# Kernel tuning notes

Hardware: AMD Instinct MI355X
Metric: run time of the kernel (lower is better)

Reference implementation:

```python
import jax, jax.numpy as jnp
import numpy as np

# Model dims (GatedAttentionLayer of Qwen3.5 ANE hybrid stack)
C = 2048      # hidden_size
H = 16        # num_attention_heads
HK = 4        # num_key_value_heads
D = 128       # head_dim
ROT = 32      # rotary_dim = head_dim * partial_rotary_factor (0.25)
S = 1024      # sequence length (prefill)
CTX = 1024    # kv cache context length
N_ATTN = 6    # number of full-attention layers -> kv_cache leading dim 2*N_ATTN
EPS = 1e-6
ROPE_THETA = 1e7


def _rotate_half(x):
    h = x.shape[-1] // 2
    return jnp.concatenate([-x[..., h:], x[..., :h]], axis=-1)


def _rms_norm(x, w, eps=EPS):
    # Qwen3.5 convention: stored weight is (w - 1), applied as (1 + weight)
    r = jax.lax.rsqrt(jnp.mean(x * x, axis=-1, keepdims=True) + eps)
    return x * r * (1.0 + w)


def setup_inputs() -> dict:
    key = jax.random.key(0)
    ks = jax.random.split(key, 6)
    hidden_states = jax.random.normal(ks[0], (1, C, 1, S), jnp.float32)
    q_proj_w = jax.random.normal(ks[1], (H * 2 * D, C), jnp.float32) * 0.02  # q + gate
    k_proj_w = jax.random.normal(ks[2], (HK * D, C), jnp.float32) * 0.02
    v_proj_w = jax.random.normal(ks[3], (HK * D, C), jnp.float32) * 0.02
    o_proj_w = jax.random.normal(ks[4], (C, H * D), jnp.float32) * 0.02
    q_norm_w = jnp.zeros((D,), jnp.float32)
    k_norm_w = jnp.zeros((D,), jnp.float32)
    kv_cache = jnp.zeros((2 * N_ATTN, HK, CTX, D), jnp.float32)
    position_ids = jnp.arange(S, dtype=jnp.int32)
    # causal mask: 0 on/below diagonal, -1e9 above
    causal_mask = jnp.where(
        jnp.arange(CTX)[None, :] <= jnp.arange(S)[:, None], 0.0, -1e9
    ).astype(jnp.float32)[None, None]  # [1,1,S,CTX]
    # RoPE tables over rotary_dim
    inv_freq = 1.0 / (ROPE_THETA ** (jnp.arange(0, ROT, 2, dtype=jnp.float32) / ROT))
    t = jnp.arange(CTX, dtype=jnp.float32)
    freqs = jnp.outer(t, inv_freq)          # [CTX, ROT//2]
    emb = jnp.concatenate([freqs, freqs], -1)  # [CTX, ROT]
    cos_cached = jnp.cos(emb)
    sin_cached = jnp.sin(emb)
    return dict(hidden_states=hidden_states, q_proj_w=q_proj_w, k_proj_w=k_proj_w,
                v_proj_w=v_proj_w, o_proj_w=o_proj_w, q_norm_w=q_norm_w,
                k_norm_w=k_norm_w, kv_cache=kv_cache, causal_mask=causal_mask,
                position_ids=position_ids, cos_cached=cos_cached,
                sin_cached=sin_cached, attn_layer_idx=0)


def reference(hidden_states, q_proj_w, k_proj_w, v_proj_w, o_proj_w,
              q_norm_w, k_norm_w, kv_cache, causal_mask, position_ids,
              cos_cached, sin_cached, attn_layer_idx):
    x = hidden_states[0, :, 0, :]                     # [C, S]
    q_raw = q_proj_w @ x                              # [H*2D, S]  (1x1 Conv2d == GEMM)
    qg = q_raw.reshape(H, 2 * D, S)
    q = jnp.transpose(qg[:, :D, :], (0, 2, 1))        # [H, S, D]
    gate = jnp.transpose(qg[:, D:, :], (0, 2, 1))     # [H, S, D]
    k = jnp.transpose((k_proj_w @ x).reshape(HK, D, S), (0, 2, 1))  # [HK, S, D]
    v = jnp.transpose((v_proj_w @ x).reshape(HK, D, S), (0, 2, 1))  # [HK, S, D]

    q = _rms_norm(q, q_norm_w)
    k = _rms_norm(k, k_norm_w)

    cos = cos_cached[position_ids]   # [S, ROT]
    sin = sin_cached[position_ids]

    def rope(t):
        rot, pas = t[..., :ROT], t[..., ROT:]
        rot = rot * cos + _rotate_half(rot) * sin
        return jnp.concatenate([rot, pas], axis=-1)

    q, k = rope(q), rope(k)

    # prefill cache write at pos_start = position_ids[0]
    k_idx = 2 * attn_layer_idx
    v_idx = k_idx + 1
    pos_start = position_ids[0]
    kv_cache = jax.lax.dynamic_update_slice(kv_cache, k[None], (k_idx, 0, pos_start, 0))
    kv_cache = jax.lax.dynamic_update_slice(kv_cache, v[None], (v_idx, 0, pos_start, 0))

    g = H // HK  # GQA repeat (expand+reshape == contiguous repeat)
    k_full = jnp.repeat(kv_cache[k_idx], g, axis=0)   # [H, CTX, D]
    v_full = jnp.repeat(kv_cache[v_idx], g, axis=0)   # [H, CTX, D]

    scale = D ** -0.5
    attn = jnp.einsum('hsd,htd->hst', q, k_full) * scale + causal_mask[0]
    attn = jax.nn.softmax(attn, axis=-1)
    out = jnp.einsum('hst,htd->hsd', attn, v_full)    # [H, S, D]
    out = out * jax.nn.sigmoid(gate)
    out = jnp.transpose(out, (0, 2, 1)).reshape(H * D, S)
    output = (o_proj_w @ out)[None, :, None, :]       # [1, C, 1, S]
    return output
```

## Files before the change

kernel.cpp:

```cpp
#include <hip/hip_runtime.h>
#include <cstdint>

#define S_LEN 1024
#define C_DIM 2048
#define NH    16
#define NHK   4
#define HD    128
#define ROT   32
#define SCALE 0.08838834764831845f

typedef __bf16 bf16x8 __attribute__((ext_vector_type(8)));
typedef float floatx4 __attribute__((ext_vector_type(4)));
typedef float floatx16 __attribute__((ext_vector_type(16)));
typedef unsigned short ushortx8 __attribute__((ext_vector_type(8)));

__device__ __forceinline__ unsigned short f2bf(float f) {
  union { float f; uint32_t u; } x; x.f = f;
  uint32_t r = (x.u + 0x7fffu + ((x.u >> 16) & 1u)) >> 16;
  return (unsigned short)r;
}
__device__ __forceinline__ float bf2f(unsigned short v) {
  union { uint32_t u; float f; } x; x.u = (uint32_t)v << 16; return x.f;
}

__device__ __forceinline__ void async_copy16(const unsigned short* g, unsigned short* l) {
  __builtin_amdgcn_global_load_lds(
      (const __attribute__((address_space(1))) void*)g,
      (__attribute__((address_space(3))) void*)l,
      16, 0, 0);
}

#define WAIT_VM(N) asm volatile("s_waitcnt vmcnt(" #N ")" ::: "memory")

__device__ __forceinline__ void bar_lds_only() {
  asm volatile("s_waitcnt lgkmcnt(0)" ::: "memory");
  __builtin_amdgcn_s_barrier();
}

__device__ __forceinline__ int swz8(int row) { return (row ^ (row >> 3)) & 7; }

__global__ __launch_bounds__(256)
void prep_kernel(const float* __restrict__ qw, const float* __restrict__ kw,
                 const float* __restrict__ vw, const float* __restrict__ ow,
                 unsigned short* __restrict__ wout,
                 const float* __restrict__ x, unsigned short* __restrict__ xT) {
  __shared__ float t[32][33];
  int bid = blockIdx.x;
  if (bid < 14336) {
    const int NQ = 4096 * 2048 / 4, NK = 512 * 2048 / 4, NV = 512 * 2048 / 4;
    int i = bid * 256 + threadIdx.x;
    const float* src; int j;
    if (i < NQ) { src = qw; j = i; }
    else if (i < NQ + NK) { src = kw; j = i - NQ; }
    else if (i < NQ + NK + NV) { src = vw; j = i - NQ - NK; }
    else { src = ow; j = i - NQ - NK - NV; }
    float4 v = ((const float4*)src)[j];
    ushort4 o;
    o.x = f2bf(v.x); o.y = f2bf(v.y); o.z = f2bf(v.z); o.w = f2bf(v.w);
    ((ushort4*)wout)[i] = o;
  } else {
    int b2 = bid - 14336;
    int st = b2 & 31, ct = b2 >> 5;
    int c = threadIdx.x & 31, rq = threadIdx.x >> 5;
#pragma unroll
    for (int i = 0; i < 4; ++i) {
      int r = rq + i * 8;
      t[r][c] = x[(size_t)(ct * 32 + r) * S_LEN + st * 32 + c];
    }
    __syncthreads();
#pragma unroll
    for (int i = 0; i < 4; ++i) {
      int r = rq + i * 8;
      xT[(size_t)(st * 32 + r) * C_DIM + ct * 32 + c] = f2bf(t[c][r]);
    }
  }
}

__device__ __forceinline__ void norm_rope_epi4(
    floatx16 (&acc)[2], float (*pp)[64],
    const float* __restrict__ w, const int* __restrict__ pos_ids,
    const float* __restrict__ cosc, const float* __restrict__ sinc,
    unsigned short* __restrict__ outp,
    int wave, int lane, int wm, int scol0) {
  int l31 = lane & 31, half = lane >> 5;
#pragma unroll
  for (int ni = 0; ni < 2; ++ni) {
    float s = 0.f;
#pragma unroll
    for (int reg = 0; reg < 16; ++reg) { float v = acc[ni][reg]; s += v * v; }
    s += __shfl_xor(s, 32);
    if (half == 0) pp[wave][ni * 32 + l31] = s;
  }
  __syncthreads();
#pragma unroll
  for (int ni = 0; ni < 2; ++ni) {
    int ci = ni * 32 + l31;
    float tot = pp[0][ci] + pp[1][ci] + pp[2][ci] + pp[3][ci];
    float rn = rsqrtf(tot * (1.0f / 128.0f) + 1e-6f);
    int scol = scol0 + ni * 32 + l31;
    int pos = pos_ids[scol];
    bool rope = (wm == 0);
#pragma unroll
    for (int g = 0; g < 4; ++g) {
      int dbase = wm + half * 4 + g * 8;
      ushort4 o;
#pragma unroll
      for (int rr = 0; rr < 4; ++rr) {
        int reg = g * 4 + rr;
        int d = dbase + rr;
        float v = acc[ni][reg] * rn * (1.0f + w[d]);
        if (rope) {
          float cv = cosc[pos * ROT + d], sv = sinc[pos * ROT + d];
          int d2 = (d < 16) ? d + 16 : d - 16;
          float pv = acc[ni][reg ^ 8] * rn * (1.0f + w[d2]);
          v = v * cv + ((d < 16) ? -pv : pv) * sv;
        }
        ((unsigned short*)&o)[rr] = f2bf(v);
      }
      *(ushort4*)&outp[(size_t)scol * HD + dbase] = o;
    }
  }
}

#define STAGE_QKV4(B_, KT)                                                     \
  { _Pragma("unroll")                                                          \
    for (int i = 0; i < 4; ++i) {                                              \
      int row = wm + i * 8 + sr;                                               \
      async_copy16(Ag + (size_t)row * C_DIM + (KT) + (sc ^ swz8(row)) * 8,     \
                   &Asm[B_][(wm + i * 8) * 64]);                               \
    }                                                                          \
    _Pragma("unroll")                                                          \
    for (int i = 0; i < 2; ++i) {                                              \
      int row = wave * 16 + i * 8 + sr;                                        \
      async_copy16(Bg + (size_t)row * C_DIM + (KT) + (sc ^ swz8(row)) * 8,     \
                   &Bsm[B_][(wave * 16 + i * 8) * 64]);                        \
    } }

__global__ __launch_bounds__(256, 3)
void gemm_qkv_fused(const unsigned short* __restrict__ A,
                    const unsigned short* __restrict__ BT,
                    const float* __restrict__ qw, const float* __restrict__ kw,
                    const int* __restrict__ pos_ids,
                    const float* __restrict__ cosc, const float* __restrict__ sinc,
                    unsigned short* __restrict__ qb, unsigned short* __restrict__ kbuf,
                    unsigned short* __restrict__ vTb, unsigned short* __restrict__ sgb) {
  __shared__ unsigned short Asm[2][128 * 64];
  __shared__ unsigned short Bsm[2][64 * 64];
  __shared__ float pp[4][64];
  int tid = threadIdx.x, wave = tid >> 6, lane = tid & 63;
  int l31 = lane & 31, half = lane >> 5;
  int wm = wave * 32;
  int m0 = blockIdx.x * 128, n0 = blockIdx.y * 64;
  int sr = lane >> 3, sc = lane & 7;
  const unsigned short* Ag = A + (size_t)m0 * C_DIM;
  const unsigned short* Bg = BT + (size_t)n0 * C_DIM;
  int aswz = swz8(wm + l31);
  int bswz0 = swz8(l31), bswz1 = swz8(32 + l31);
  floatx16 acc[2];
  acc[0] = (floatx16)0.f; acc[1] = (floatx16)0.f;

  STAGE_QKV4(0, 0)
  STAGE_QKV4(1, 64)

  for (int t = 0; t < 32; ++t) {
    int b = t & 1;
    if (t < 31) { WAIT_VM(6); } else { WAIT_VM(0); }
    __builtin_amdgcn_s_barrier();
#pragma unroll
    for (int kb = 0; kb < 4; ++kb) {
      int c2 = (kb << 1) | half;
      bf16x8 av  = *(const bf16x8*)&Asm[b][(wm + l31) * 64 + ((c2 ^ aswz) << 3)];
      bf16x8 b0v = *(const bf16x8*)&Bsm[b][l31 * 64 + ((c2 ^ bswz0) << 3)];
      bf16x8 b1v = *(const bf16x8*)&Bsm[b][(32 + l31) * 64 + ((c2 ^ bswz1) << 3)];
      acc[0] = __builtin_amdgcn_mfma_f32_32x32x16_bf16(av, b0v, acc[0], 0, 0, 0);
      acc[1] = __builtin_amdgcn_mfma_f32_32x32x16_bf16(av, b1v, acc[1], 0, 0, 0);
    }
    bar_lds_only();
    if (t < 30) STAGE_QKV4(b, (t + 2) * 64)
  }

  int scol0 = n0;
  int ty = blockIdx.x;
  if (ty < 32) {
    int h = ty >> 1;
    if ((ty & 1) == 0) {
      norm_rope_epi4(acc, pp, qw, pos_ids, cosc, sinc,
                     qb + (size_t)h * S_LEN * HD, wave, lane, wm, scol0);
    } else {
#pragma unroll
      for (int ni = 0; ni < 2; ++ni) {
        int scol = scol0 + ni * 32 + l31;
#pragma unroll
        for (int g = 0; g < 4; ++g) {
          int dbase = wm + half * 4 + g * 8;
          ushort4 o;
#pragma unroll
          for (int rr = 0; rr < 4; ++rr)
            ((unsigned short*)&o)[rr] = f2bf(1.0f / (1.0f + __expf(-acc[ni][g * 4 + rr])));
          *(ushort4*)&sgb[((size_t)h * S_LEN + scol) * HD + dbase] = o;
        }
      }
    }
  } else if (ty < 36) {
    int hk = ty - 32;
    norm_rope_epi4(acc, pp, kw, pos_ids, cosc, sinc,
                   kbuf + (size_t)hk * S_LEN * HD, wave, lane, wm, scol0);
  } else {
    int hk = ty - 36;
#pragma unroll
    for (int ni = 0; ni < 2; ++ni)
#pragma unroll
      for (int reg = 0; reg < 16; ++reg) {
        int d = wm + (reg & 3) + 8 * (reg >> 2) + 4 * half;
        vTb[(size_t)hk * HD * S_LEN + (size_t)d * S_LEN + scol0 + ni * 32 + l31] =
            f2bf(acc[ni][reg]);
      }
  }
}

#define STAGE_O2(B_, KT)                                                       \
  { _Pragma("unroll")                                                          \
    for (int i = 0; i < 4; ++i) {                                              \
      int row = wm + i * 8 + sr;                                               \
      async_copy16(Ag + (size_t)row * C_DIM + (KT) + (sc ^ swz8(row)) * 8,     \
                   &Asm[B_][(wm + i * 8) * 64]);                               \
    }                                                                          \
    _Pragma("unroll")                                                          \
    for (int i = 0; i < 4; ++i) {                                              \
      int row = wm + i * 8 + sr;                                               \
      async_copy16(Bg + (size_t)row * C_DIM + (KT) + (sc ^ swz8(row)) * 8,     \
                   &Bsm[B_][(wm + i * 8) * 64]);                               \
    } }

__global__ __launch_bounds__(128, 2)
void gemm_oproj(const unsigned short* __restrict__ A,
                const unsigned short* __restrict__ BT,
                float* __restrict__ C) {
  __shared__ unsigned short Asm[2][64 * 64];
  __shared__ unsigned short Bsm[2][64 * 64];
  int tid = threadIdx.x, wave = tid >> 6, lane = tid & 63;
  int l31 = lane & 31, half = lane >> 5;
  int wm = wave * 32;
  int m0 = blockIdx.x * 64, n0 = blockIdx.y * 64;
  int sr = lane >> 3, sc = lane & 7;
  const unsigned short* Ag = A + (size_t)m0 * C_DIM;
  const unsigned short* Bg = BT + (size_t)n0 * C_DIM;
  int aswz = swz8(wm + l31);
  int bswz0 = swz8(l31), bswz1 = swz8(32 + l31);
  floatx16 acc[2];
  acc[0] = (floatx16)0.f; acc[1] = (floatx16)0.f;

  STAGE_O2(0, 0)
  STAGE_O2(1, 64)

  for (int t = 0; t < 32; ++t) {
    int b = t & 1;
    if (t < 31) { WAIT_VM(8); } else { WAIT_VM(0); }
    __builtin_amdgcn_s_barrier();
#pragma unroll
    for (int kb = 0; kb < 4; ++kb) {
      int c2 = (kb << 1) | half;
      bf16x8 av  = *(const bf16x8*)&Asm[b][(wm + l31) * 64 + ((c2 ^ aswz) << 3)];
      bf16x8 b0v = *(const bf16x8*)&Bsm[b][l31 * 64 + ((c2 ^ bswz0) << 3)];
      bf16x8 b1v = *(const bf16x8*)&Bsm[b][(32 + l31) * 64 + ((c2 ^ bswz1) << 3)];
      acc[0] = __builtin_amdgcn_mfma_f32_32x32x16_bf16(av, b0v, acc[0], 0, 0, 0);
      acc[1] = __builtin_amdgcn_mfma_f32_32x32x16_bf16(av, b1v, acc[1], 0, 0, 0);
    }
    bar_lds_only();
    if (t < 30) STAGE_O2(b, (t + 2) * 64)
  }

#pragma unroll
  for (int ni = 0; ni < 2; ++ni)
#pragma unroll
    for (int reg = 0; reg < 16; ++reg) {
      int row = m0 + wm + (reg & 3) + 8 * (reg >> 2) + 4 * half;
      C[(size_t)row * S_LEN + n0 + ni * 32 + l31] = acc[ni][reg];
    }
}

__global__ __launch_bounds__(256)
void attn_kernel(const unsigned short* __restrict__ qb,
                 const unsigned short* __restrict__ kbuf,
                 const unsigned short* __restrict__ vTb,
                 float* __restrict__ pm, float* __restrict__ pl,
                 float* __restrict__ pO0, float* __restrict__ pO1) {
  __shared__ __align__(16) unsigned short Ks[64 * 128];
  __shared__ __align__(16) unsigned short Vs[128 * 64];
  __shared__ __align__(16) unsigned short Ps[4][16][72];
  int h = blockIdx.x, qt = blockIdx.y, ch = blockIdx.z;
  int t0 = ch * 4;
  if (t0 > qt) return;
  int t1 = min(qt, t0 + 3);
  int s0 = qt * 64;
  int hk = h >> 2;
  int tid = threadIdx.x, wave = tid >> 6, lane = tid & 63;
  int l16 = lane & 15, quad = lane >> 4;
  int lsw = l16 & 7;

  const unsigned short* qg = qb + ((size_t)(h * S_LEN + s0 + wave * 16 + l16)) * HD;
  bf16x8 qfr[4];
#pragma unroll
  for (int kb = 0; kb < 4; ++kb)
    qfr[kb] = *(const bf16x8*)(qg + kb * 32 + quad * 8);

  float m_r[4], l_r[4];
#pragma unroll
  for (int r = 0; r < 4; ++r) { m_r[r] = -1e30f; l_r[r] = 0.f; }
  floatx4 acc_o[8];
#pragma unroll
  for (int i = 0; i < 8; ++i) acc_o[i] = (floatx4)0.f;
  int srow_base = s0 + wave * 16 + quad * 4;

  const unsigned short* kg0 = kbuf + (size_t)hk * S_LEN * HD;
  const unsigned short* vg0 = vTb + (size_t)hk * HD * S_LEN;

  int kr4 = lane >> 4, kc16 = lane & 15;
  int vr8 = lane >> 3, vc8 = lane & 7;

  for (int t = t0; t <= t1; ++t) {
    int jt = t * 64;
#pragma unroll
    for (int i = 0; i < 4; ++i) {
      int rbase = wave * 16 + i * 4;
      int row = rbase + kr4;
      int cs = kc16 ^ (row & 7);
      async_copy16(kg0 + (size_t)(jt + row) * HD + cs * 8, Ks + rbase * 128);
    }
#pragma unroll
    for (int i = 0; i < 4; ++i) {
      int rbase = wave * 32 + i * 8;
      int row = rbase + vr8;
      int cs = vc8 ^ (row & 7);
      async_copy16(vg0 + (size_t)row * S_LEN + jt + cs * 8, Vs + rbase * 64);
    }
    __syncthreads();

    floatx4 acc_s[4];
#pragma unroll
    for (int ni = 0; ni < 4; ++ni) acc_s[ni] = (floatx4)0.f;
#pragma unroll
    for (int kb = 0; kb < 4; ++kb) {
#pragma unroll
      for (int ni = 0; ni < 4; ++ni) {
        int cl = (kb * 4 + quad) ^ lsw;
        bf16x8 bk = *(const bf16x8*)&Ks[(ni * 16 + l16) * 128 + cl * 8];
        acc_s[ni] = __builtin_amdgcn_mfma_f32_16x16x32_bf16(qfr[kb], bk, acc_s[ni], 0, 0, 0);
      }
    }

    bool diag = (t == qt);
    float alpha[4];
#pragma unroll
    for (int r = 0; r < 4; ++r) {
      float scv[4];
      float mx = -1e30f;
#pragma unroll
      for (int ni = 0; ni < 4; ++ni) {
        float sv = acc_s[ni][r] * SCALE;
        if (diag) {
          int jg = jt + ni * 16 + l16;
          if (jg > srow_base + r) sv = -1e30f;
        }
        scv[ni] = sv;
        mx = fmaxf(mx, sv);
      }
#pragma unroll
      for (int off = 8; off; off >>= 1) mx = fmaxf(mx, __shfl_xor(mx, off, 16));
      float mnew = fmaxf(m_r[r], mx);
      float psv = 0.f;
#pragma unroll
      for (int ni = 0; ni < 4; ++ni) {
        float pv = (scv[ni] > -1e29f) ? __expf(scv[ni] - mnew) : 0.f;
        Ps[wave][quad * 4 + r][ni * 16 + l16] = f2bf(pv);
        psv += pv;
      }
#pragma unroll
      for (int off = 8; off; off >>= 1) psv += __shfl_xor(psv, off, 16);
      alpha[r] = __expf(m_r[r] - mnew);
      m_r[r] = mnew;
      l_r[r] = l_r[r] * alpha[r] + psv;
    }
#pragma unroll
    for (int i = 0; i < 8; ++i)
#pragma unroll
      for (int r = 0; r < 4; ++r) acc_o[i][r] *= alpha[r];
    __threadfence_block();

#pragma unroll
    for (int kb2 = 0; kb2 < 2; ++kb2) {
      bf16x8 ap = *(const bf16x8*)&Ps[wave][l16][kb2 * 32 + quad * 8];
#pragma unroll
      for (int ni2 = 0; ni2 < 8; ++ni2) {
        int cl = (kb2 * 4 + quad) ^ lsw;
        bf16x8 bv = *(const bf16x8*)&Vs[(ni2 * 16 + l16) * 64 + cl * 8];
        acc_o[ni2] = __builtin_amdgcn_mfma_f32_16x16x32_bf16(ap, bv, acc_o[ni2], 0, 0, 0);
      }
    }
    __syncthreads();
  }

  size_t pmbase = ((size_t)(h * 16 + qt) * 4 + ch) * 64;
  float* pOp = (ch < 2) ? pO0 + ((size_t)(h * 16 + qt) * 2 + ch) * 8192
                        : pO1 + ((size_t)(h * 16 + qt) * 2 + (ch - 2)) * 8192;
#pragma unroll
  for (int r = 0; r < 4; ++r) {
    int rrow = wave * 16 + quad * 4 + r;
    if (l16 == 0) { pm[pmbase + rrow] = m_r[r]; pl[pmbase + rrow] = l_r[r]; }
#pragma unroll
    for (int ni2 = 0; ni2 < 8; ++ni2)
      pOp[rrow * 128 + ni2 * 16 + l16] = acc_o[ni2][r];
  }
}

__global__ __launch_bounds__(256)
void attn_merge(const float* __restrict__ pm, const float* __restrict__ pl,
                const float* __restrict__ pO0, const float* __restrict__ pO1,
                const unsigned short* __restrict__ sgb,
                unsigned short* __restrict__ outT) {
  int h = blockIdx.x, qt = blockIdx.y;
  int vc = (qt >> 2) + 1;
  size_t base = (size_t)(h * 16 + qt) * 4;
  int lane32 = threadIdx.x & 31, rb = threadIdx.x >> 5;
  int d = lane32 * 4;
#pragma unroll
  for (int rr = 0; rr < 8; ++rr) {
    int row = rr * 8 + rb;
    float M = -1e30f;
    for (int c = 0; c < vc; ++c) M = fmaxf(M, pm[(base + c) * 64 + row]);
    float L = 0.f;
    floatx4 acc = (floatx4)0.f;
    for (int c = 0; c < vc; ++c) {
      float w = __expf(pm[(base + c) * 64 + row] - M);
      L += w * pl[(base + c) * 64 + row];
      const float* Op = (c < 2) ? pO0 + ((size_t)(h * 16 + qt) * 2 + c) * 8192
                                : pO1 + ((size_t)(h * 16 + qt) * 2 + (c - 2)) * 8192;
      floatx4 o = *(const floatx4*)&Op[row * 128 + d];
#pragma unroll
      for (int j = 0; j < 4; ++j) acc[j] += w * o[j];
    }
    float inv = 1.0f / L;
    int s = qt * 64 + row;
    ushort4 sg4 = *(const ushort4*)&sgb[((size_t)h * S_LEN + s) * HD + d];
    ushort4 out4;
#pragma unroll
    for (int j = 0; j < 4; ++j)
      ((unsigned short*)&out4)[j] = f2bf(acc[j] * inv * bf2f(((unsigned short*)&sg4)[j]));
    *(ushort4*)&outT[(size_t)s * (NH * HD) + h * HD + d] = out4;
  }
}

extern "C" void kernel_launch(void* const* d_in, const int* in_sizes, int n_in,
                              void* d_out, int out_size, void* d_ws, size_t ws_size,
                              hipStream_t stream) {
  const float* hs       = (const float*)d_in[0];
  const float* q_proj_w = (const float*)d_in[1];
  const float* k_proj_w = (const float*)d_in[2];
  const float* v_proj_w = (const float*)d_in[3];
  const float* o_proj_w = (const float*)d_in[4];
  const float* q_norm_w = (const float*)d_in[5];
  const float* k_norm_w = (const float*)d_in[6];
  const int*   pos_ids  = (const int*)d_in[9];
  const float* cos_c    = (const float*)d_in[10];
  const float* sin_c    = (const float*)d_in[11];
  float* out = (float*)d_out;

  char* ws = (char*)d_ws;
  unsigned short* wqkv = (unsigned short*)(ws + 0);
  unsigned short* wo   = (unsigned short*)(ws + 20971520);
  unsigned short* xT   = (unsigned short*)(ws + 29360128);
  unsigned short* qb   = (unsigned short*)(ws + 33554432);
  unsigned short* kbuf = (unsigned short*)(ws + 37748736);
  unsigned short* vTb  = (unsigned short*)(ws + 38797312);
  unsigned short* sgb  = (unsigned short*)(ws + 39845888);
  unsigned short* aoT  = (unsigned short*)(ws + 44040192);
  float*          pO0  = (float*)(ws + 0);
  float*          pO1  = (float*)(ws + 48234496);
  float*          pm   = (float*)(ws + 65011712);
  float*          pl   = (float*)(ws + 65273856);

  prep_kernel<<<14336 + 2048, 256, 0, stream>>>(q_proj_w, k_proj_w, v_proj_w, o_proj_w,
                                                wqkv, hs, xT);
  gemm_qkv_fused<<<dim3(40, 16), 256, 0, stream>>>(wqkv, xT, q_norm_w, k_norm_w,
                                                   pos_ids, cos_c, sin_c,
                                                   qb, kbuf, vTb, sgb);
  attn_kernel<<<dim3(16, 16, 4), 256, 0, stream>>>(qb, kbuf, vTb, pm, pl, pO0, pO1);
  attn_merge<<<dim3(16, 16), 256, 0, stream>>>(pm, pl, pO0, pO1, sgb, aoT);
  gemm_oproj<<<dim3(32, 16), 128, 0, stream>>>(wo, aoT, out);
}
```

Before: 231.4 us.

## Fuse attention merge into attention kernel via last-block atomic counter

Removes the separate attn_merge launch. The last of the split-KV blocks finishing a (head, query-tile) pair, detected with an atomic counter, performs the softmax merge and gating in place. Query tiles with a single KV chunk now write the gated, normalized output directly and skip the partial buffers. The counters are zeroed in prep_kernel, which adds a threadfence and atomic per block and a serial merge tail on the last block.

```diff
diff --git a/kernel.cpp b/kernel.cpp
--- a/kernel.cpp
+++ b/kernel.cpp
@@ -43,9 +43,11 @@
 void prep_kernel(const float* __restrict__ qw, const float* __restrict__ kw,
                  const float* __restrict__ vw, const float* __restrict__ ow,
                  unsigned short* __restrict__ wout,
-                 const float* __restrict__ x, unsigned short* __restrict__ xT) {
+                 const float* __restrict__ x, unsigned short* __restrict__ xT,
+                 int* __restrict__ cnt) {
   __shared__ float t[32][33];
   int bid = blockIdx.x;
+  if (bid == 0 && threadIdx.x < 256) cnt[threadIdx.x] = 0;
   if (bid < 14336) {
     const int NQ = 4096 * 2048 / 4, NK = 512 * 2048 / 4, NV = 512 * 2048 / 4;
     int i = bid * 256 + threadIdx.x;
@@ -283,15 +285,20 @@
 void attn_kernel(const unsigned short* __restrict__ qb,
                  const unsigned short* __restrict__ kbuf,
                  const unsigned short* __restrict__ vTb,
+                 const unsigned short* __restrict__ sgb,
+                 unsigned short* __restrict__ outT,
                  float* __restrict__ pm, float* __restrict__ pl,
-                 float* __restrict__ pO0, float* __restrict__ pO1) {
+                 float* __restrict__ pO0, float* __restrict__ pO1,
+                 int* __restrict__ cnt) {
   __shared__ __align__(16) unsigned short Ks[64 * 128];
   __shared__ __align__(16) unsigned short Vs[128 * 64];
   __shared__ __align__(16) unsigned short Ps[4][16][72];
+  __shared__ int is_last;
   int h = blockIdx.x, qt = blockIdx.y, ch = blockIdx.z;
   int t0 = ch * 4;
   if (t0 > qt) return;
   int t1 = min(qt, t0 + 3);
+  int vc = (qt >> 2) + 1;
   int s0 = qt * 64;
   int hk = h >> 2;
   int tid = threadIdx.x, wave = tid >> 6, lane = tid & 63;
@@ -400,6 +407,22 @@
     __syncthreads();
   }
 
+  if (vc == 1) {
+#pragma unroll
+    for (int r = 0; r < 4; ++r) {
+      int s = srow_base + r;
+      float inv = 1.0f / l_r[r];
+      const unsigned short* sgp = sgb + ((size_t)h * S_LEN + s) * HD;
+      unsigned short* op = outT + (size_t)s * (NH * HD) + h * HD;
+#pragma unroll
+      for (int ni2 = 0; ni2 < 8; ++ni2) {
+        int d = ni2 * 16 + l16;
+        op[d] = f2bf(acc_o[ni2][r] * inv * bf2f(sgp[d]));
+      }
+    }
+    return;
+  }
+
   size_t pmbase = ((size_t)(h * 16 + qt) * 4 + ch) * 64;
   float* pOp = (ch < 2) ? pO0 + ((size_t)(h * 16 + qt) * 2 + ch) * 8192
                         : pO1 + ((size_t)(h * 16 + qt) * 2 + (ch - 2)) * 8192;
@@ -411,17 +434,19 @@
     for (int ni2 = 0; ni2 < 8; ++ni2)
       pOp[rrow * 128 + ni2 * 16 + l16] = acc_o[ni2][r];
   }
-}
-
-__global__ __launch_bounds__(256)
-void attn_merge(const float* __restrict__ pm, const float* __restrict__ pl,
-                const float* __restrict__ pO0, const float* __restrict__ pO1,
-                const unsigned short* __restrict__ sgb,
-                unsigned short* __restrict__ outT) {
-  int h = blockIdx.x, qt = blockIdx.y;
-  int vc = (qt >> 2) + 1;
+
+  __threadfence();
+  __syncthreads();
+  if (tid == 0) {
+    int old = atomicAdd(&cnt[h * 16 + qt], 1);
+    is_last = (old == vc - 1) ? 1 : 0;
+  }
+  __syncthreads();
+  if (!is_last) return;
+  __threadfence();
+
   size_t base = (size_t)(h * 16 + qt) * 4;
-  int lane32 = threadIdx.x & 31, rb = threadIdx.x >> 5;
+  int lane32 = tid & 31, rb = tid >> 5;
   int d = lane32 * 4;
 #pragma unroll
   for (int rr = 0; rr < 8; ++rr) {
@@ -478,13 +503,14 @@
   float*          pO1  = (float*)(ws + 48234496);
   float*          pm   = (float*)(ws + 65011712);
   float*          pl   = (float*)(ws + 65273856);
+  int*            cnt  = (int*)(ws + 65536000);
 
   prep_kernel<<<14336 + 2048, 256, 0, stream>>>(q_proj_w, k_proj_w, v_proj_w, o_proj_w,
-                                                wqkv, hs, xT);
+                                                wqkv, hs, xT, cnt);
   gemm_qkv_fused<<<dim3(40, 16), 256, 0, stream>>>(wqkv, xT, q_norm_w, k_norm_w,
                                                    pos_ids, cos_c, sin_c,
                                                    qb, kbuf, vTb, sgb);
-  attn_kernel<<<dim3(16, 16, 4), 256, 0, stream>>>(qb, kbuf, vTb, pm, pl, pO0, pO1);
-  attn_merge<<<dim3(16, 16), 256, 0, stream>>>(pm, pl, pO0, pO1, sgb, aoT);
+  attn_kernel<<<dim3(16, 16, 4), 256, 0, stream>>>(qb, kbuf, vTb, sgb, aoT,
+                                                   pm, pl, pO0, pO1, cnt);
   gemm_oproj<<<dim3(32, 16), 128, 0, stream>>>(wo, aoT, out);
 }
```

New measurement: 328.2 us. 41.8% more time.

## Halve split-KV chunks and finalize single-chunk query tiles inside attention kernel

Applied to the files above, without the earlier changes.

Each attention block now covers up to 8 KV tiles instead of 4, so there are at most two KV chunks per query tile. Query tiles with only one chunk (the first half) apply the softmax normalization and sigmoid gate and write bf16 output directly, skipping the partial-result round trip. The merge kernel now runs only on the second half of query tiles and combines exactly two partials. The aim is less partial-buffer traffic and merge work, at the cost of fewer blocks and a longer critical path per block, which can hurt load balance and occupancy.

```diff
diff --git a/kernel.cpp b/kernel.cpp
--- a/kernel.cpp
+++ b/kernel.cpp
@@ -283,15 +283,18 @@
 void attn_kernel(const unsigned short* __restrict__ qb,
                  const unsigned short* __restrict__ kbuf,
                  const unsigned short* __restrict__ vTb,
+                 const unsigned short* __restrict__ sgb,
+                 unsigned short* __restrict__ outT,
                  float* __restrict__ pm, float* __restrict__ pl,
                  float* __restrict__ pO0, float* __restrict__ pO1) {
   __shared__ __align__(16) unsigned short Ks[64 * 128];
   __shared__ __align__(16) unsigned short Vs[128 * 64];
   __shared__ __align__(16) unsigned short Ps[4][16][72];
   int h = blockIdx.x, qt = blockIdx.y, ch = blockIdx.z;
-  int t0 = ch * 4;
+  int t0 = ch * 8;
   if (t0 > qt) return;
-  int t1 = min(qt, t0 + 3);
+  int t1 = min(qt, t0 + 7);
+  int vc = (qt >= 8) ? 2 : 1;
   int s0 = qt * 64;
   int hk = h >> 2;
   int tid = threadIdx.x, wave = tid >> 6, lane = tid & 63;
@@ -400,13 +403,28 @@
     __syncthreads();
   }
 
-  size_t pmbase = ((size_t)(h * 16 + qt) * 4 + ch) * 64;
-  float* pOp = (ch < 2) ? pO0 + ((size_t)(h * 16 + qt) * 2 + ch) * 8192
-                        : pO1 + ((size_t)(h * 16 + qt) * 2 + (ch - 2)) * 8192;
+  if (vc == 1) {
+#pragma unroll
+    for (int r = 0; r < 4; ++r) {
+      int s = srow_base + r;
+      float inv = 1.0f / l_r[r];
+      const unsigned short* sgp = sgb + ((size_t)h * S_LEN + s) * HD;
+      unsigned short* op = outT + (size_t)s * (NH * HD) + h * HD;
+#pragma unroll
+      for (int ni2 = 0; ni2 < 8; ++ni2) {
+        int d = ni2 * 16 + l16;
+        op[d] = f2bf(acc_o[ni2][r] * inv * bf2f(sgp[d]));
+      }
+    }
+    return;
+  }
+
+  size_t pr = (size_t)(h * 16 + qt);
+  float* pOp = ((ch == 0) ? pO0 : pO1) + pr * 8192;
 #pragma unroll
   for (int r = 0; r < 4; ++r) {
     int rrow = wave * 16 + quad * 4 + r;
-    if (l16 == 0) { pm[pmbase + rrow] = m_r[r]; pl[pmbase + rrow] = l_r[r]; }
+    if (l16 == 0) { pm[(pr * 2 + ch) * 64 + rrow] = m_r[r]; pl[(pr * 2 + ch) * 64 + rrow] = l_r[r]; }
 #pragma unroll
     for (int ni2 = 0; ni2 < 8; ++ni2)
       pOp[rrow * 128 + ni2 * 16 + l16] = acc_o[ni2][r];
@@ -418,34 +436,31 @@
                 const float* __restrict__ pO0, const float* __restrict__ pO1,
                 const unsigned short* __restrict__ sgb,
                 unsigned short* __restrict__ outT) {
-  int h = blockIdx.x, qt = blockIdx.y;
-  int vc = (qt >> 2) + 1;
-  size_t base = (size_t)(h * 16 + qt) * 4;
+  int h = blockIdx.x, qt = blockIdx.y + 8;
+  size_t pr = (size_t)(h * 16 + qt);
+  const float* O0 = pO0 + pr * 8192;
+  const float* O1 = pO1 + pr * 8192;
   int lane32 = threadIdx.x & 31, rb = threadIdx.x >> 5;
   int d = lane32 * 4;
 #pragma unroll
   for (int rr = 0; rr < 8; ++rr) {
     int row = rr * 8 + rb;
-    float M = -1e30f;
-    for (int c = 0; c < vc; ++c) M = fmaxf(M, pm[(base + c) * 64 + row]);
-    float L = 0.f;
-    floatx4 acc = (floatx4)0.f;
-    for (int c = 0; c < vc; ++c) {
-      float w = __expf(pm[(base + c) * 64 + row] - M);
-      L += w * pl[(base + c) * 64 + row];
-      const float* Op = (c < 2) ? pO0 + ((size_t)(h * 16 + qt) * 2 + c) * 8192
-                                : pO1 + ((size_t)(h * 16 + qt) * 2 + (c - 2)) * 8192;
-      floatx4 o = *(const floatx4*)&Op[row * 128 + d];
-#pragma unroll
-      for (int j = 0; j < 4; ++j) acc[j] += w * o[j];
-    }
+    float m0 = pm[(pr * 2 + 0) * 64 + row], l0 = pl[(pr * 2 + 0) * 64 + row];
+    float m1 = pm[(pr * 2 + 1) * 64 + row], l1 = pl[(pr * 2 + 1) * 64 + row];
+    float M = fmaxf(m0, m1);
+    float w0 = __expf(m0 - M), w1 = __expf(m1 - M);
+    float L = w0 * l0 + w1 * l1;
     float inv = 1.0f / L;
+    floatx4 o0 = *(const floatx4*)&O0[row * 128 + d];
+    floatx4 o1 = *(const floatx4*)&O1[row * 128 + d];
     int s = qt * 64 + row;
     ushort4 sg4 = *(const ushort4*)&sgb[((size_t)h * S_LEN + s) * HD + d];
     ushort4 out4;
 #pragma unroll
-    for (int j = 0; j < 4; ++j)
-      ((unsigned short*)&out4)[j] = f2bf(acc[j] * inv * bf2f(((unsigned short*)&sg4)[j]));
+    for (int j = 0; j < 4; ++j) {
+      float v = (o0[j] * w0 + o1[j] * w1) * inv;
+      ((unsigned short*)&out4)[j] = f2bf(v * bf2f(((unsigned short*)&sg4)[j]));
+    }
     *(ushort4*)&outT[(size_t)s * (NH * HD) + h * HD + d] = out4;
   }
 }
@@ -477,14 +492,15 @@
   float*          pO0  = (float*)(ws + 0);
   float*          pO1  = (float*)(ws + 48234496);
   float*          pm   = (float*)(ws + 65011712);
-  float*          pl   = (float*)(ws + 65273856);
+  float*          pl   = (float*)(ws + 65142784);
 
   prep_kernel<<<14336 + 2048, 256, 0, stream>>>(q_proj_w, k_proj_w, v_proj_w, o_proj_w,
                                                 wqkv, hs, xT);
   gemm_qkv_fused<<<dim3(40, 16), 256, 0, stream>>>(wqkv, xT, q_norm_w, k_norm_w,
                                                    pos_ids, cos_c, sin_c,
                                                    qb, kbuf, vTb, sgb);
-  attn_kernel<<<dim3(16, 16, 4), 256, 0, stream>>>(qb, kbuf, vTb, pm, pl, pO0, pO1);
-  attn_merge<<<dim3(16, 16), 256, 0, stream>>>(pm, pl, pO0, pO1, sgb, aoT);
+  attn_kernel<<<dim3(16, 16, 2), 256, 0, stream>>>(qb, kbuf, vTb, sgb, aoT,
+                                                   pm, pl, pO0, pO1);
+  attn_merge<<<dim3(16, 8), 256, 0, stream>>>(pm, pl, pO0, pO1, sgb, aoT);
   gemm_oproj<<<dim3(32, 16), 128, 0, stream>>>(wo, aoT, out);
 }
```

Result: faster. 226.1 us, median of 2 (-2.3%).
